# Kernel tuning notes

Hardware: AMD Instinct MI355X
Metric: run time of the kernel (lower is better)

The kernel has to match this reference:

```python
import jax, jax.numpy as jnp
import numpy as np

N_IN = 1024
N_OUT = 2048
EMBED_DIM = 1024  # == n_in so multi-layer path type-checks
LAYERS = 2
T, B = 128, 64


def setup_inputs() -> dict:
    key = jax.random.key(0)
    ks = jax.random.split(key, 8)
    s_in = 1.0 / np.sqrt(N_IN)
    s_out = 1.0 / np.sqrt(N_OUT)
    return {
        "xt": jax.random.normal(ks[0], (T, B, N_IN), jnp.float32),
        "ct_forward": jnp.zeros((LAYERS, B, N_OUT), jnp.float32),
        # weights stored [in, out] (transposed vs torch Linear)
        "Wx": jax.random.uniform(ks[1], (N_IN, N_OUT), jnp.float32, -s_in, s_in),
        "Wf": jax.random.uniform(ks[2], (N_IN, N_OUT), jnp.float32, -s_in, s_in),
        "bf": jnp.zeros((N_OUT,), jnp.float32),
        "Wr": jax.random.uniform(ks[3], (N_IN, N_OUT), jnp.float32, -s_in, s_in),
        "br": jnp.zeros((N_OUT,), jnp.float32),
        "Wcx": jax.random.uniform(ks[4], (N_IN, N_OUT), jnp.float32, -s_in, s_in),
        "bcx": jnp.zeros((N_OUT,), jnp.float32),
        "Wcl": jax.random.uniform(ks[5], (N_OUT, EMBED_DIM), jnp.float32, -s_out, s_out),
        "bcl": jnp.zeros((EMBED_DIM,), jnp.float32),
    }


def _one_layer(x, c0, Wx, Wf, bf, Wr, br, Wcx, bcx):
    # x: [T, B, n_in]; c0: [B, n_out]
    # batch all projections over time (compute-dense GEMMs)
    xp = jnp.einsum("tbi,io->tbo", x, Wx)                     # x_t projection
    f = jax.nn.sigmoid(jnp.einsum("tbi,io->tbo", x, Wf) + bf)  # forget gate
    r = jax.nn.sigmoid(jnp.einsum("tbi,io->tbo", x, Wr) + br)  # reset gate
    cx = jnp.einsum("tbi,io->tbo", x, Wcx) + bcx               # highway path

    def step(c, inp):
        f_t, xp_t = inp
        c_new = f_t * c + (1.0 - f_t) * xp_t
        return c_new, c_new

    c_last, c_seq = jax.lax.scan(step, c0, (f, xp))
    h = r * jnp.tanh(c_seq) + (1.0 - r) * cx
    return h, c_last


def reference(xt, ct_forward, Wx, Wf, bf, Wr, br, Wcx, bcx, Wcl, bcl):
    x = xt
    c_last = ct_forward[0]
    for l in range(LAYERS):
        if x.shape[2] == N_OUT:  # layers >= 2: project back to embed_dim (= n_in)
            x = jnp.einsum("tbo,oe->tbe", x, Wcl) + bcl
        x, c_last = _one_layer(x, ct_forward[l], Wx, Wf, bf, Wr, br, Wcx, bcx)
    # dropout p=0.0 -> identity
    return x, c_last
```

## Files before the change

kernel.cpp:

```cpp
#include <hip/hip_runtime.h>

#define TT 128
#define BB 64
#define NIN 1024
#define NOUT 2048
#define MR (TT*BB)

typedef unsigned short u16;
typedef __attribute__((ext_vector_type(8))) __bf16 bf16x8;
typedef __attribute__((ext_vector_type(4))) float f32x4;
typedef __attribute__((ext_vector_type(8))) unsigned short u16x8;

static __device__ __forceinline__ u16 f2bf(float f) {
    union { float f; unsigned u; } v; v.f = f;
    unsigned r = v.u + 0x7fffu + ((v.u >> 16) & 1u);
    return (u16)(r >> 16);
}
static __device__ __forceinline__ float bf2f(u16 x) {
    union { unsigned u; float f; } v; v.u = ((unsigned)x) << 16;
    return v.f;
}

__global__ void k_cvt_chunk(const float* __restrict__ s, u16* __restrict__ d, int M_, int K_) {
    __shared__ float t[64][33];
    int m0 = blockIdx.x * 64, k0 = blockIdx.y * 32;
    int ml = threadIdx.x >> 3, kl = (threadIdx.x & 7) * 4;
    #pragma unroll
    for (int p = 0; p < 2; ++p) {
        float4 v = *(const float4*)&s[(size_t)(m0 + ml + p * 32) * K_ + k0 + kl];
        t[ml + p * 32][kl] = v.x; t[ml + p * 32][kl + 1] = v.y;
        t[ml + p * 32][kl + 2] = v.z; t[ml + p * 32][kl + 3] = v.w;
    }
    __syncthreads();
    int q = threadIdx.x >> 6, row = threadIdx.x & 63;
    u16x8 o;
    #pragma unroll
    for (int j = 0; j < 8; ++j) o[j] = f2bf(t[row][q * 8 + j]);
    *(u16x8*)&d[(((size_t)(k0 >> 3) + q) * M_ + m0 + row) * 8] = o;
}

__global__ void k_wT_chunk(const float* __restrict__ s, u16* __restrict__ d,
                           int K_, int N_, int OUTM, int row_off) {
    __shared__ float t[32][65];
    int k0 = blockIdx.y * 32, n0 = blockIdx.x * 64;
    int kl = threadIdx.x >> 6, nl = threadIdx.x & 63;
    #pragma unroll
    for (int p = 0; p < 8; ++p)
        t[kl + p * 4][nl] = s[(size_t)(k0 + kl + p * 4) * N_ + n0 + nl];
    __syncthreads();
    int q = threadIdx.x >> 6, row = threadIdx.x & 63;
    u16x8 o;
    #pragma unroll
    for (int j = 0; j < 8; ++j) o[j] = f2bf(t[q * 8 + j][row]);
    *(u16x8*)&d[(((size_t)(k0 >> 3) + q) * OUTM + row_off + n0 + row) * 8] = o;
}

__global__ void k_bias_pack(const float* __restrict__ bf_, const float* __restrict__ br_,
                            const float* __restrict__ bcx_, float* __restrict__ ball) {
    int i = blockIdx.x * 256 + threadIdx.x;
    int g = i >> 11, n = i & 2047;
    float v = 0.f;
    if (g == 1) v = bf_[n];
    else if (g == 2) v = br_[n];
    else if (g == 3) v = bcx_[n];
    ball[i] = v;
}

#define GLL16(SRC, DST) __builtin_amdgcn_global_load_lds( \
    (const __attribute__((address_space(1))) void*)(SRC), \
    (__attribute__((address_space(3))) void*)(DST), 16, 0, 0)
#define SBAR() __builtin_amdgcn_s_barrier()
#define SCHED0() __builtin_amdgcn_sched_barrier(0)

template<int WM>
__global__ __launch_bounds__(512) void k_gemm_c(
    const u16* __restrict__ A, const u16* __restrict__ BT,
    const float* __restrict__ bias, u16* __restrict__ outG, u16* __restrict__ outC,
    int M, int NB, int K)
{
    constexpr int BM = WM * 32;
    constexpr int BUF = BM * 32 + 8192;
    constexpr int AL = (WM == 8) ? 2 : 1;
    __shared__ __align__(16) u16 L[4 * BUF];

    const int tid = threadIdx.x;
    const int w = tid >> 6, lane = tid & 63;
    const int wr = w >> 2, wc = w & 3;
    const int lr = lane & 15, kq = lane >> 4;
    const int m0 = blockIdx.y * BM, n0 = blockIdx.x * 256;
    const int nk = K >> 5;

    const u16* aSrc[AL]; int aDst[AL];
    #pragma unroll
    for (int l = 0; l < AL; ++l) {
        int tc = tid + l * 512;
        int q = tc / BM, row = tc % BM;
        aSrc[l] = A + ((size_t)q * M + m0 + row) * 8;
        aDst[l] = (w * 64 + l * 512) * 8;
    }
    const u16* bSrc[2]; int bDst[2];
    #pragma unroll
    for (int l = 0; l < 2; ++l) {
        int tc = tid + l * 512;
        int q = tc >> 8, row = tc & 255;
        bSrc[l] = BT + ((size_t)q * NB + n0 + row) * 8;
        bDst[l] = BM * 32 + (w * 64 + l * 512) * 8;
    }
    const size_t aStep = (size_t)32 * M;
    const size_t bStep = (size_t)32 * NB;

    const int rdA = wr * (WM * 16) + lr;
    const int rdB = wc * 64 + lr;

    f32x4 acc[WM][4] = {};

    #pragma unroll
    for (int p = 0; p < 3; ++p) {
        #pragma unroll
        for (int l = 0; l < AL; ++l) GLL16(aSrc[l] + (size_t)p * aStep, &L[p * BUF + aDst[l]]);
        #pragma unroll
        for (int l = 0; l < 2; ++l)  GLL16(bSrc[l] + (size_t)p * bStep, &L[p * BUF + bDst[l]]);
    }
    if (WM == 8) asm volatile("s_waitcnt vmcnt(8)" ::: "memory");
    else         asm volatile("s_waitcnt vmcnt(6)" ::: "memory");
    SBAR(); SCHED0();

    for (int kt = 0; kt < nk; ++kt) {
        const int bb = (kt & 3) * BUF;
        const int sb = ((kt + 3) & 3) * BUF;
        const bool st = (kt + 3) < nk;
        const size_t sOffA = (size_t)(kt + 3) * aStep;
        const size_t sOffB = (size_t)(kt + 3) * bStep;

        bf16x8 aF[4], bF[4];
        #pragma unroll
        for (int i = 0; i < 4; ++i)
            aF[i] = *(const bf16x8*)&L[bb + (kq * BM + rdA + i * 16) * 8];
        #pragma unroll
        for (int j = 0; j < 4; ++j)
            bF[j] = *(const bf16x8*)&L[bb + BM * 32 + (kq * 256 + rdB + j * 16) * 8];
        if (st) {
            #pragma unroll
            for (int l = 0; l < AL; ++l) GLL16(aSrc[l] + sOffA, &L[sb + aDst[l]]);
        }
        SBAR();
        __builtin_amdgcn_s_setprio(1);
        #pragma unroll
        for (int i = 0; i < 4; ++i)
            #pragma unroll
            for (int j = 0; j < 4; ++j)
                acc[i][j] = __builtin_amdgcn_mfma_f32_16x16x32_bf16(aF[i], bF[j], acc[i][j], 0, 0, 0);
        __builtin_amdgcn_s_setprio(0);

        if constexpr (WM == 8) {
            SBAR();
            bf16x8 aG[4];
            #pragma unroll
            for (int i = 0; i < 4; ++i)
                aG[i] = *(const bf16x8*)&L[bb + (kq * BM + rdA + 64 + i * 16) * 8];
            if (st) {
                #pragma unroll
                for (int l = 0; l < 2; ++l) GLL16(bSrc[l] + sOffB, &L[sb + bDst[l]]);
            }
            SBAR();
            __builtin_amdgcn_s_setprio(1);
            #pragma unroll
            for (int i = 0; i < 4; ++i)
                #pragma unroll
                for (int j = 0; j < 4; ++j)
                    acc[i + 4][j] = __builtin_amdgcn_mfma_f32_16x16x32_bf16(aG[i], bF[j], acc[i + 4][j], 0, 0, 0);
            __builtin_amdgcn_s_setprio(0);
            if (kt + 3 < nk)      asm volatile("s_waitcnt vmcnt(8)" ::: "memory");
            else if (kt + 2 < nk) asm volatile("s_waitcnt vmcnt(4)" ::: "memory");
            else                  asm volatile("s_waitcnt vmcnt(0)" ::: "memory");
        } else {
            if (st) {
                #pragma unroll
                for (int l = 0; l < 2; ++l) GLL16(bSrc[l] + sOffB, &L[sb + bDst[l]]);
            }
            if (kt + 3 < nk)      asm volatile("s_waitcnt vmcnt(6)" ::: "memory");
            else if (kt + 2 < nk) asm volatile("s_waitcnt vmcnt(3)" ::: "memory");
            else                  asm volatile("s_waitcnt vmcnt(0)" ::: "memory");
        }
        SBAR(); SCHED0();
    }

    const size_t GM2 = (size_t)M << 11;
    #pragma unroll
    for (int i = 0; i < WM; ++i) {
        int r0 = m0 + wr * (WM * 16) + i * 16 + kq * 4;
        #pragma unroll
        for (int j = 0; j < 4; ++j) {
            int gc = n0 + wc * 64 + j * 16 + lr;
            float bv = bias[gc];
            if (outG) {
                int g = gc >> 11;
                bool sig = (g == 1 || g == 2);
                size_t base = (size_t)g * GM2 + (size_t)(gc & 2047);
                #pragma unroll
                for (int q = 0; q < 4; ++q) {
                    float v = acc[i][j][q] + bv;
                    if (sig) v = 1.f / (1.f + __expf(-v));
                    outG[base + (size_t)(r0 + q) * 2048] = f2bf(v);
                }
            } else {
                size_t base = ((size_t)(gc >> 3) * M) * 8 + (size_t)(gc & 7);
                #pragma unroll
                for (int q = 0; q < 4; ++q)
                    outC[base + (size_t)(r0 + q) * 8] = f2bf(acc[i][j][q] + bv);
            }
        }
    }
}

__global__ void k_scan(const u16* __restrict__ G, const float* __restrict__ c0,
                       u16* __restrict__ hb, float* __restrict__ hf,
                       float* __restrict__ cout)
{
    int idx = blockIdx.x * 256 + threadIdx.x;
    int b = idx >> 11, n = idx & 2047;
    float c = c0[idx];
    const size_t GM = (size_t)MR * 2048;
    const size_t hcBase = ((size_t)(n >> 3) * MR) * 8 + (size_t)(n & 7);
    for (int t = 0; t < TT; ++t) {
        int m = t * BB + b;
        size_t p = ((size_t)m << 11) + (size_t)n;
        float xp = bf2f(G[p]);
        float f  = bf2f(G[GM + p]);
        float r  = bf2f(G[2 * GM + p]);
        float cx = bf2f(G[3 * GM + p]);
        c = f * c + (1.f - f) * xp;
        float h = r * tanhf(c) + (1.f - r) * cx;
        if (hb) hb[hcBase + (size_t)m * 8] = f2bf(h);
        if (hf) hf[p] = h;
    }
    if (cout) cout[idx] = c;
}

extern "C" void kernel_launch(void* const* d_in, const int* in_sizes, int n_in,
                              void* d_out, int out_size, void* d_ws, size_t ws_size,
                              hipStream_t stream)
{
    const float* xt  = (const float*)d_in[0];
    const float* ctf = (const float*)d_in[1];
    const float* Wx  = (const float*)d_in[2];
    const float* Wf  = (const float*)d_in[3];
    const float* bfp = (const float*)d_in[4];
    const float* Wr  = (const float*)d_in[5];
    const float* brp = (const float*)d_in[6];
    const float* Wcx = (const float*)d_in[7];
    const float* bcx = (const float*)d_in[8];
    const float* Wcl = (const float*)d_in[9];
    const float* bcl = (const float*)d_in[10];
    float* out = (float*)d_out;

    char* ws = (char*)d_ws;
    u16* x0 = (u16*)ws;       ws += (size_t)MR * NIN * 2;
    u16* x2 = (u16*)ws;       ws += (size_t)MR * NIN * 2;
    u16* h1 = (u16*)ws;       ws += (size_t)MR * NOUT * 2;
    u16* WTall = (u16*)ws;    ws += (size_t)4 * NOUT * NIN * 2;
    u16* WclT = (u16*)ws;     ws += (size_t)NIN * NOUT * 2;
    float* ball = (float*)ws; ws += (size_t)4 * NOUT * 4;
    u16* G = (u16*)ws;        ws += (size_t)4 * MR * NOUT * 2;

    k_cvt_chunk<<<dim3(MR / 64, NIN / 32), 256, 0, stream>>>(xt, x0, MR, NIN);
    k_wT_chunk<<<dim3(NOUT / 64, NIN / 32), 256, 0, stream>>>(Wx,  WTall, NIN, NOUT, 4 * NOUT, 0 * NOUT);
    k_wT_chunk<<<dim3(NOUT / 64, NIN / 32), 256, 0, stream>>>(Wf,  WTall, NIN, NOUT, 4 * NOUT, 1 * NOUT);
    k_wT_chunk<<<dim3(NOUT / 64, NIN / 32), 256, 0, stream>>>(Wr,  WTall, NIN, NOUT, 4 * NOUT, 2 * NOUT);
    k_wT_chunk<<<dim3(NOUT / 64, NIN / 32), 256, 0, stream>>>(Wcx, WTall, NIN, NOUT, 4 * NOUT, 3 * NOUT);
    k_wT_chunk<<<dim3(NIN / 64, NOUT / 32), 256, 0, stream>>>(Wcl, WclT, NOUT, NIN, NIN, 0);
    k_bias_pack<<<32, 256, 0, stream>>>(bfp, brp, bcx, ball);

    k_gemm_c<8><<<dim3(32, 32), 512, 0, stream>>>(x0, WTall, ball, G, (u16*)nullptr, MR, 4 * NOUT, NIN);
    k_scan<<<(BB * NOUT) / 256, 256, 0, stream>>>(G, ctf, h1, (float*)nullptr, (float*)nullptr);

    k_gemm_c<4><<<dim3(NIN / 256, MR / 128), 512, 0, stream>>>(h1, WclT, bcl, (u16*)nullptr, x2, MR, NIN, NOUT);

    k_gemm_c<8><<<dim3(32, 32), 512, 0, stream>>>(x2, WTall, ball, G, (u16*)nullptr, MR, 4 * NOUT, NIN);
    k_scan<<<(BB * NOUT) / 256, 256, 0, stream>>>(G, ctf + (size_t)BB * NOUT, (u16*)nullptr, out, out + (size_t)MR * NOUT);
}
```

Before: 512.8 us.

## Restructure GEMM main loop with register double-buffering and one barrier per tile

Splits the templated GEMM into two specialized kernels and restructures the K loop so LDS fragments for the next k-tile are loaded into a second register set while the current tile's MFMAs run. This leaves one barrier per iteration instead of three. It also adds an XCD-style workgroup swizzle of block indices to improve L2 locality, and sets launch_bounds occupancy to 2. The extra fragment registers raise register pressure and could force spills or reduce occupancy. Reading the next buffer right after issuing prefetches also relies on the 4-stage ring staying correct with only one barrier.

```diff
diff --git a/kernel.cpp b/kernel.cpp
--- a/kernel.cpp
+++ b/kernel.cpp
@@ -72,143 +72,215 @@
 #define SBAR() __builtin_amdgcn_s_barrier()
 #define SCHED0() __builtin_amdgcn_sched_barrier(0)
 
-template<int WM>
-__global__ __launch_bounds__(512) void k_gemm_c(
+__global__ __launch_bounds__(512, 2) void k_gemm8(
     const u16* __restrict__ A, const u16* __restrict__ BT,
-    const float* __restrict__ bias, u16* __restrict__ outG, u16* __restrict__ outC,
+    const float* __restrict__ bias, u16* __restrict__ outG,
     int M, int NB, int K)
 {
-    constexpr int BM = WM * 32;
+    constexpr int BM = 256;
     constexpr int BUF = BM * 32 + 8192;
-    constexpr int AL = (WM == 8) ? 2 : 1;
     __shared__ __align__(16) u16 L[4 * BUF];
 
     const int tid = threadIdx.x;
     const int w = tid >> 6, lane = tid & 63;
     const int wr = w >> 2, wc = w & 3;
     const int lr = lane & 15, kq = lane >> 4;
-    const int m0 = blockIdx.y * BM, n0 = blockIdx.x * 256;
+    const int gx = gridDim.x;
+    const int nwg = gx * gridDim.y;
+    const int flat = blockIdx.y * gx + blockIdx.x;
+    const int swz = (flat & 7) * (nwg >> 3) + (flat >> 3);
+    const int m0 = (swz / gx) * BM, n0 = (swz % gx) * 256;
     const int nk = K >> 5;
 
-    const u16* aSrc[AL]; int aDst[AL];
-    #pragma unroll
-    for (int l = 0; l < AL; ++l) {
-        int tc = tid + l * 512;
-        int q = tc / BM, row = tc % BM;
-        aSrc[l] = A + ((size_t)q * M + m0 + row) * 8;
-        aDst[l] = (w * 64 + l * 512) * 8;
-    }
-    const u16* bSrc[2]; int bDst[2];
+    const u16* aSrc[2]; int aDst[2];
     #pragma unroll
     for (int l = 0; l < 2; ++l) {
         int tc = tid + l * 512;
-        int q = tc >> 8, row = tc & 255;
-        bSrc[l] = BT + ((size_t)q * NB + n0 + row) * 8;
+        aSrc[l] = A + ((size_t)(tc >> 8) * M + m0 + (tc & 255)) * 8;
+        aDst[l] = (w * 64 + l * 512) * 8;
+    }
+    const u16* bSrc[2]; int bDst[2];
+    #pragma unroll
+    for (int l = 0; l < 2; ++l) {
+        int tc = tid + l * 512;
+        bSrc[l] = BT + ((size_t)(tc >> 8) * NB + n0 + (tc & 255)) * 8;
         bDst[l] = BM * 32 + (w * 64 + l * 512) * 8;
     }
     const size_t aStep = (size_t)32 * M;
     const size_t bStep = (size_t)32 * NB;
-
-    const int rdA = wr * (WM * 16) + lr;
+    const int rdA = wr * 128 + lr;
     const int rdB = wc * 64 + lr;
 
-    f32x4 acc[WM][4] = {};
+    f32x4 acc[8][4] = {};
+    bf16x8 aP0[4], bP0[4], aP1[4], bP1[4];
 
     #pragma unroll
     for (int p = 0; p < 3; ++p) {
         #pragma unroll
-        for (int l = 0; l < AL; ++l) GLL16(aSrc[l] + (size_t)p * aStep, &L[p * BUF + aDst[l]]);
-        #pragma unroll
-        for (int l = 0; l < 2; ++l)  GLL16(bSrc[l] + (size_t)p * bStep, &L[p * BUF + bDst[l]]);
-    }
-    if (WM == 8) asm volatile("s_waitcnt vmcnt(8)" ::: "memory");
-    else         asm volatile("s_waitcnt vmcnt(6)" ::: "memory");
+        for (int l = 0; l < 2; ++l) GLL16(aSrc[l] + (size_t)p * aStep, &L[p * BUF + aDst[l]]);
+        #pragma unroll
+        for (int l = 0; l < 2; ++l) GLL16(bSrc[l] + (size_t)p * bStep, &L[p * BUF + bDst[l]]);
+    }
+    asm volatile("s_waitcnt vmcnt(4)" ::: "memory");
     SBAR(); SCHED0();
-
-    for (int kt = 0; kt < nk; ++kt) {
-        const int bb = (kt & 3) * BUF;
-        const int sb = ((kt + 3) & 3) * BUF;
-        const bool st = (kt + 3) < nk;
-        const size_t sOffA = (size_t)(kt + 3) * aStep;
-        const size_t sOffB = (size_t)(kt + 3) * bStep;
-
-        bf16x8 aF[4], bF[4];
-        #pragma unroll
-        for (int i = 0; i < 4; ++i)
-            aF[i] = *(const bf16x8*)&L[bb + (kq * BM + rdA + i * 16) * 8];
-        #pragma unroll
-        for (int j = 0; j < 4; ++j)
-            bF[j] = *(const bf16x8*)&L[bb + BM * 32 + (kq * 256 + rdB + j * 16) * 8];
-        if (st) {
-            #pragma unroll
-            for (int l = 0; l < AL; ++l) GLL16(aSrc[l] + sOffA, &L[sb + aDst[l]]);
-        }
-        SBAR();
-        __builtin_amdgcn_s_setprio(1);
-        #pragma unroll
-        for (int i = 0; i < 4; ++i)
-            #pragma unroll
-            for (int j = 0; j < 4; ++j)
-                acc[i][j] = __builtin_amdgcn_mfma_f32_16x16x32_bf16(aF[i], bF[j], acc[i][j], 0, 0, 0);
-        __builtin_amdgcn_s_setprio(0);
-
-        if constexpr (WM == 8) {
-            SBAR();
-            bf16x8 aG[4];
-            #pragma unroll
-            for (int i = 0; i < 4; ++i)
-                aG[i] = *(const bf16x8*)&L[bb + (kq * BM + rdA + 64 + i * 16) * 8];
-            if (st) {
-                #pragma unroll
-                for (int l = 0; l < 2; ++l) GLL16(bSrc[l] + sOffB, &L[sb + bDst[l]]);
-            }
-            SBAR();
-            __builtin_amdgcn_s_setprio(1);
-            #pragma unroll
-            for (int i = 0; i < 4; ++i)
-                #pragma unroll
-                for (int j = 0; j < 4; ++j)
-                    acc[i + 4][j] = __builtin_amdgcn_mfma_f32_16x16x32_bf16(aG[i], bF[j], acc[i + 4][j], 0, 0, 0);
-            __builtin_amdgcn_s_setprio(0);
-            if (kt + 3 < nk)      asm volatile("s_waitcnt vmcnt(8)" ::: "memory");
-            else if (kt + 2 < nk) asm volatile("s_waitcnt vmcnt(4)" ::: "memory");
-            else                  asm volatile("s_waitcnt vmcnt(0)" ::: "memory");
-        } else {
-            if (st) {
-                #pragma unroll
-                for (int l = 0; l < 2; ++l) GLL16(bSrc[l] + sOffB, &L[sb + bDst[l]]);
-            }
-            if (kt + 3 < nk)      asm volatile("s_waitcnt vmcnt(6)" ::: "memory");
-            else if (kt + 2 < nk) asm volatile("s_waitcnt vmcnt(3)" ::: "memory");
-            else                  asm volatile("s_waitcnt vmcnt(0)" ::: "memory");
-        }
-        SBAR(); SCHED0();
-    }
+    #pragma unroll
+    for (int i = 0; i < 4; ++i) aP0[i] = *(const bf16x8*)&L[(kq * BM + rdA + i * 16) * 8];
+    #pragma unroll
+    for (int j = 0; j < 4; ++j) bP0[j] = *(const bf16x8*)&L[BM * 32 + (kq * 256 + rdB + j * 16) * 8];
+
+#define ITER8(KT, CUR, NXT) { \
+    const int kt_ = (KT); \
+    const int bb = (kt_ & 3) * BUF; \
+    const int tn = (kt_ + 1 < nk) ? kt_ + 1 : nk - 1; \
+    const int nb = (tn & 3) * BUF; \
+    bf16x8 aG[4]; \
+    _Pragma("unroll") for (int i = 0; i < 4; ++i) \
+        aG[i] = *(const bf16x8*)&L[bb + (kq * BM + rdA + 64 + i * 16) * 8]; \
+    if (kt_ + 3 < nk) { \
+        const size_t sa = (size_t)(kt_ + 3) * aStep, sb_ = (size_t)(kt_ + 3) * bStep; \
+        const int wb = ((kt_ + 3) & 3) * BUF; \
+        _Pragma("unroll") for (int l = 0; l < 2; ++l) GLL16(aSrc[l] + sa, &L[wb + aDst[l]]); \
+        _Pragma("unroll") for (int l = 0; l < 2; ++l) GLL16(bSrc[l] + sb_, &L[wb + bDst[l]]); \
+    } \
+    __builtin_amdgcn_s_setprio(1); \
+    _Pragma("unroll") for (int i = 0; i < 4; ++i) \
+        _Pragma("unroll") for (int j = 0; j < 4; ++j) \
+            acc[i][j] = __builtin_amdgcn_mfma_f32_16x16x32_bf16(aP##CUR[i], bP##CUR[j], acc[i][j], 0, 0, 0); \
+    _Pragma("unroll") for (int i = 0; i < 4; ++i) \
+        aP##NXT[i] = *(const bf16x8*)&L[nb + (kq * BM + rdA + i * 16) * 8]; \
+    _Pragma("unroll") for (int j = 0; j < 4; ++j) \
+        bP##NXT[j] = *(const bf16x8*)&L[nb + BM * 32 + (kq * 256 + rdB + j * 16) * 8]; \
+    _Pragma("unroll") for (int i = 0; i < 4; ++i) \
+        _Pragma("unroll") for (int j = 0; j < 4; ++j) \
+            acc[i + 4][j] = __builtin_amdgcn_mfma_f32_16x16x32_bf16(aG[i], bP##CUR[j], acc[i + 4][j], 0, 0, 0); \
+    __builtin_amdgcn_s_setprio(0); \
+    asm volatile("s_waitcnt vmcnt(4)" ::: "memory"); \
+    SBAR(); SCHED0(); }
+
+    for (int kt4 = 0; kt4 < nk; kt4 += 4) {
+        ITER8(kt4 + 0, 0, 1);
+        ITER8(kt4 + 1, 1, 0);
+        ITER8(kt4 + 2, 0, 1);
+        ITER8(kt4 + 3, 1, 0);
+    }
+#undef ITER8
 
     const size_t GM2 = (size_t)M << 11;
     #pragma unroll
-    for (int i = 0; i < WM; ++i) {
-        int r0 = m0 + wr * (WM * 16) + i * 16 + kq * 4;
+    for (int i = 0; i < 8; ++i) {
+        int r0 = m0 + wr * 128 + i * 16 + kq * 4;
         #pragma unroll
         for (int j = 0; j < 4; ++j) {
             int gc = n0 + wc * 64 + j * 16 + lr;
             float bv = bias[gc];
-            if (outG) {
-                int g = gc >> 11;
-                bool sig = (g == 1 || g == 2);
-                size_t base = (size_t)g * GM2 + (size_t)(gc & 2047);
-                #pragma unroll
-                for (int q = 0; q < 4; ++q) {
-                    float v = acc[i][j][q] + bv;
-                    if (sig) v = 1.f / (1.f + __expf(-v));
-                    outG[base + (size_t)(r0 + q) * 2048] = f2bf(v);
-                }
-            } else {
-                size_t base = ((size_t)(gc >> 3) * M) * 8 + (size_t)(gc & 7);
-                #pragma unroll
-                for (int q = 0; q < 4; ++q)
-                    outC[base + (size_t)(r0 + q) * 8] = f2bf(acc[i][j][q] + bv);
+            int g = gc >> 11;
+            bool sig = (g == 1 || g == 2);
+            size_t base = (size_t)g * GM2 + (size_t)(gc & 2047);
+            #pragma unroll
+            for (int q = 0; q < 4; ++q) {
+                float v = acc[i][j][q] + bv;
+                if (sig) v = 1.f / (1.f + __expf(-v));
+                outG[base + (size_t)(r0 + q) * 2048] = f2bf(v);
             }
+        }
+    }
+}
+
+__global__ __launch_bounds__(512, 2) void k_gemm4(
+    const u16* __restrict__ A, const u16* __restrict__ BT,
+    const float* __restrict__ bias, u16* __restrict__ outC,
+    int M, int NB, int K)
+{
+    constexpr int BM = 128;
+    constexpr int BUF = BM * 32 + 8192;
+    __shared__ __align__(16) u16 L[4 * BUF];
+
+    const int tid = threadIdx.x;
+    const int w = tid >> 6, lane = tid & 63;
+    const int wr = w >> 2, wc = w & 3;
+    const int lr = lane & 15, kq = lane >> 4;
+    const int gx = gridDim.x;
+    const int nwg = gx * gridDim.y;
+    const int flat = blockIdx.y * gx + blockIdx.x;
+    const int swz = (flat & 7) * (nwg >> 3) + (flat >> 3);
+    const int m0 = (swz / gx) * BM, n0 = (swz % gx) * 256;
+    const int nk = K >> 5;
+
+    const u16* aSrc1; int aDst1;
+    {
+        int q = tid >> 7, row = tid & 127;
+        aSrc1 = A + ((size_t)q * M + m0 + row) * 8;
+        aDst1 = (w * 64) * 8;
+    }
+    const u16* bSrc[2]; int bDst[2];
+    #pragma unroll
+    for (int l = 0; l < 2; ++l) {
+        int tc = tid + l * 512;
+        bSrc[l] = BT + ((size_t)(tc >> 8) * NB + n0 + (tc & 255)) * 8;
+        bDst[l] = BM * 32 + (w * 64 + l * 512) * 8;
+    }
+    const size_t aStep = (size_t)32 * M;
+    const size_t bStep = (size_t)32 * NB;
+    const int rdA = wr * 64 + lr;
+    const int rdB = wc * 64 + lr;
+
+    f32x4 acc[4][4] = {};
+    bf16x8 aP0[4], bP0[4], aP1[4], bP1[4];
+
+    #pragma unroll
+    for (int p = 0; p < 3; ++p) {
+        GLL16(aSrc1 + (size_t)p * aStep, &L[p * BUF + aDst1]);
+        #pragma unroll
+        for (int l = 0; l < 2; ++l) GLL16(bSrc[l] + (size_t)p * bStep, &L[p * BUF + bDst[l]]);
+    }
+    asm volatile("s_waitcnt vmcnt(3)" ::: "memory");
+    SBAR(); SCHED0();
+    #pragma unroll
+    for (int i = 0; i < 4; ++i) aP0[i] = *(const bf16x8*)&L[(kq * BM + rdA + i * 16) * 8];
+    #pragma unroll
+    for (int j = 0; j < 4; ++j) bP0[j] = *(const bf16x8*)&L[BM * 32 + (kq * 256 + rdB + j * 16) * 8];
+
+#define ITER4(KT, CUR, NXT) { \
+    const int kt_ = (KT); \
+    const int tn = (kt_ + 1 < nk) ? kt_ + 1 : nk - 1; \
+    const int nb = (tn & 3) * BUF; \
+    if (kt_ + 3 < nk) { \
+        const size_t sa = (size_t)(kt_ + 3) * aStep, sb_ = (size_t)(kt_ + 3) * bStep; \
+        const int wb = ((kt_ + 3) & 3) * BUF; \
+        GLL16(aSrc1 + sa, &L[wb + aDst1]); \
+        _Pragma("unroll") for (int l = 0; l < 2; ++l) GLL16(bSrc[l] + sb_, &L[wb + bDst[l]]); \
+    } \
+    __builtin_amdgcn_s_setprio(1); \
+    _Pragma("unroll") for (int i = 0; i < 4; ++i) \
+        _Pragma("unroll") for (int j = 0; j < 4; ++j) \
+            acc[i][j] = __builtin_amdgcn_mfma_f32_16x16x32_bf16(aP##CUR[i], bP##CUR[j], acc[i][j], 0, 0, 0); \
+    _Pragma("unroll") for (int i = 0; i < 4; ++i) \
+        aP##NXT[i] = *(const bf16x8*)&L[nb + (kq * BM + rdA + i * 16) * 8]; \
+    _Pragma("unroll") for (int j = 0; j < 4; ++j) \
+        bP##NXT[j] = *(const bf16x8*)&L[nb + BM * 32 + (kq * 256 + rdB + j * 16) * 8]; \
+    __builtin_amdgcn_s_setprio(0); \
+    asm volatile("s_waitcnt vmcnt(3)" ::: "memory"); \
+    SBAR(); SCHED0(); }
+
+    for (int kt4 = 0; kt4 < nk; kt4 += 4) {
+        ITER4(kt4 + 0, 0, 1);
+        ITER4(kt4 + 1, 1, 0);
+        ITER4(kt4 + 2, 0, 1);
+        ITER4(kt4 + 3, 1, 0);
+    }
+#undef ITER4
+
+    #pragma unroll
+    for (int i = 0; i < 4; ++i) {
+        int r0 = m0 + wr * 64 + i * 16 + kq * 4;
+        #pragma unroll
+        for (int j = 0; j < 4; ++j) {
+            int gc = n0 + wc * 64 + j * 16 + lr;
+            float bv = bias[gc];
+            size_t base = ((size_t)(gc >> 3) * M) * 8 + (size_t)(gc & 7);
+            #pragma unroll
+            for (int q = 0; q < 4; ++q)
+                outC[base + (size_t)(r0 + q) * 8] = f2bf(acc[i][j][q] + bv);
         }
     }
 }
@@ -271,11 +343,11 @@
     k_wT_chunk<<<dim3(NIN / 64, NOUT / 32), 256, 0, stream>>>(Wcl, WclT, NOUT, NIN, NIN, 0);
     k_bias_pack<<<32, 256, 0, stream>>>(bfp, brp, bcx, ball);
 
-    k_gemm_c<8><<<dim3(32, 32), 512, 0, stream>>>(x0, WTall, ball, G, (u16*)nullptr, MR, 4 * NOUT, NIN);
+    k_gemm8<<<dim3(32, 32), 512, 0, stream>>>(x0, WTall, ball, G, MR, 4 * NOUT, NIN);
     k_scan<<<(BB * NOUT) / 256, 256, 0, stream>>>(G, ctf, h1, (float*)nullptr, (float*)nullptr);
 
-    k_gemm_c<4><<<dim3(NIN / 256, MR / 128), 512, 0, stream>>>(h1, WclT, bcl, (u16*)nullptr, x2, MR, NIN, NOUT);
-
-    k_gemm_c<8><<<dim3(32, 32), 512, 0, stream>>>(x2, WTall, ball, G, (u16*)nullptr, MR, 4 * NOUT, NIN);
+    k_gemm4<<<dim3(NIN / 256, MR / 128), 512, 0, stream>>>(h1, WclT, bcl, x2, MR, NIN, NOUT);
+
+    k_gemm8<<<dim3(32, 32), 512, 0, stream>>>(x2, WTall, ball, G, MR, 4 * NOUT, NIN);
     k_scan<<<(BB * NOUT) / 256, 256, 0, stream>>>(G, ctf + (size_t)BB * NOUT, (u16*)nullptr, out, out + (size_t)MR * NOUT);
 }
```

New measurement: 470.2 us. 1.09x faster.
